# Performance work log

Measured on AMD Instinct MI355X. Metric: run time of the kernel, lower is better.

Reference implementation:

```python
import jax, jax.numpy as jnp
import numpy as np

N_NODES = 20000
N_EDGES = 320000
N_GRAPHS = 256
HIDDEN = 128
L = 4
NUM_ATOM = 28
NUM_BOND = 4
AVG_LOG = float(np.log(17.0))  # avg degree 16 -> avg_d['log']
EPS = 1e-5


def setup_inputs() -> dict:
    key = jax.random.key(0)
    ks = jax.random.split(key, 16)
    D = HIDDEN
    return {
        "x": jax.random.randint(ks[0], (N_NODES,), 0, NUM_ATOM, dtype=jnp.int32),
        "batch": jnp.sort(jax.random.randint(ks[1], (N_NODES,), 0, N_GRAPHS, dtype=jnp.int32)),
        "edge_index": jax.random.randint(ks[2], (2, N_EDGES), 0, N_NODES, dtype=jnp.int32),
        "snorm_n": jax.random.uniform(ks[3], (N_NODES, 1), dtype=jnp.float32),
        "edge_attr": jax.random.randint(ks[4], (N_EDGES,), 0, NUM_BOND, dtype=jnp.int32),
        "atom_emb": jax.random.normal(ks[5], (NUM_ATOM, D), jnp.float32) * 0.1,
        "bond_emb": jax.random.normal(ks[6], (NUM_BOND, D), jnp.float32) * 0.1,
        "pre_W": jax.random.normal(ks[7], (L, 3 * D, D), jnp.float32) / np.sqrt(3 * D),
        "pre_b": jnp.zeros((L, D), jnp.float32),
        "post_W": jax.random.normal(ks[8], (L, 13 * D, D), jnp.float32) / np.sqrt(13 * D),
        "post_b": jnp.zeros((L, D), jnp.float32),
        "mix_W": jax.random.normal(ks[9], (L, D, D), jnp.float32) / np.sqrt(D),
        "mix_b": jnp.zeros((L, D), jnp.float32),
        "bn_gamma": jnp.ones((L, D), jnp.float32),
        "bn_beta": jnp.zeros((L, D), jnp.float32),
        "r_W1": jax.random.normal(ks[10], (D, D // 2), jnp.float32) / np.sqrt(D),
        "r_b1": jnp.zeros((D // 2,), jnp.float32),
        "r_W2": jax.random.normal(ks[11], (D // 2, D // 4), jnp.float32) / np.sqrt(D // 2),
        "r_b2": jnp.zeros((D // 4,), jnp.float32),
        "r_W3": jax.random.normal(ks[12], (D // 4, 1), jnp.float32) / np.sqrt(D // 4),
        "r_b3": jnp.zeros((1,), jnp.float32),
    }


def _pna_forward(x, batch, edge_index, snorm_n, edge_attr,
                 atom_emb, bond_emb, pre_W, pre_b, post_W, post_b,
                 mix_W, mix_b, bn_gamma, bn_beta,
                 r_W1, r_b1, r_W2, r_b2, r_W3, r_b3):
    src, dst = edge_index[0], edge_index[1]
    h = atom_emb[x]                          # [N, D]
    e = bond_emb[edge_attr]                  # [E, D]
    # in-degree and PNA degree scalers (computed once)
    d = jax.ops.segment_sum(jnp.ones((src.shape[0],), h.dtype), dst, N_NODES)
    has_nb = (d > 0)[:, None]
    d_safe = jnp.maximum(d, 1.0)[:, None]
    logd = jnp.log1p(d)[:, None]
    amp = logd / AVG_LOG                     # amplification scaler
    att = AVG_LOG / jnp.maximum(logd, EPS)   # attenuation scaler
    for l in range(L):
        h_in = h
        # pretrans on edges: FC(cat(h_dst, h_src, e)) with LeakyReLU
        m = jnp.concatenate([h[dst], h[src], e], axis=-1)            # [E, 3D]
        m = jax.nn.leaky_relu(m @ pre_W[l] + pre_b[l])               # [E, D]
        # aggregators: mean, max, min, std
        mean = jax.ops.segment_sum(m, dst, N_NODES) / d_safe
        mean_sq = jax.ops.segment_sum(m * m, dst, N_NODES) / d_safe
        std = jnp.where(has_nb, jnp.sqrt(jax.nn.relu(mean_sq - mean * mean) + EPS), 0.0)
        mx = jnp.where(has_nb, jax.ops.segment_max(m, dst, N_NODES), 0.0)
        mn = jnp.where(has_nb, jax.ops.segment_min(m, dst, N_NODES), 0.0)
        agg = jnp.concatenate([mean, mx, mn, std], axis=-1)          # [N, 4D]
        agg = jnp.concatenate([agg, agg * amp, agg * att], axis=-1)  # [N, 12D]
        # posttrans FC on cat(h, agg) + mixing FC
        ph = jax.nn.leaky_relu(jnp.concatenate([h, agg], axis=-1) @ post_W[l] + post_b[l])
        ph = jax.nn.leaky_relu(ph @ mix_W[l] + mix_b[l])
        ph = ph * snorm_n                    # graph_norm
        mu = ph.mean(axis=0)                 # BatchNorm (training-mode stats)
        var = ph.var(axis=0)
        ph = bn_gamma[l] * (ph - mu) * jax.lax.rsqrt(var + EPS) + bn_beta[l]
        h = h_in + ph                        # residual
    # global mean pool per graph
    cnt = jax.ops.segment_sum(jnp.ones((x.shape[0],), h.dtype), batch, N_GRAPHS)
    g = jax.ops.segment_sum(h, batch, N_GRAPHS) / jnp.maximum(cnt, 1.0)[:, None]
    # MLPReadout: D -> D/2 -> D/4 -> 1 with ReLU
    g = jax.nn.relu(g @ r_W1 + r_b1)
    g = jax.nn.relu(g @ r_W2 + r_b2)
    return g @ r_W3 + r_b3                   # [B, 1]


def reference(x, batch, edge_index, snorm_n, edge_attr,
              atom_emb, bond_emb, pre_W, pre_b, post_W, post_b,
              mix_W, mix_b, bn_gamma, bn_beta,
              r_W1, r_b1, r_W2, r_b2, r_W3, r_b3):
    return _pna_forward(x, batch, edge_index, snorm_n, edge_attr,
                        atom_emb, bond_emb, pre_W, pre_b, post_W, post_b,
                        mix_W, mix_b, bn_gamma, bn_beta,
                        r_W1, r_b1, r_W2, r_b2, r_W3, r_b3)
```

## Files before the change

kernel.cpp:

```cpp
#include <hip/hip_runtime.h>
#include <math.h>

#define N_NODES 20000
#define N_EDGES 320000
#define N_GRAPHS 256
#define HID 128
#define NLAYERS 4
#define AVG_LOG 2.833213344056216f
#define EPS 1e-5f
#define MB64 313
#define NPAD 20032
#define SCANB 20
#define PITCH 40

typedef __attribute__((ext_vector_type(8))) short short8;
typedef __attribute__((ext_vector_type(4))) float f32x4;

static __device__ __forceinline__ float leaky(float v){ return v > 0.f ? v : 0.01f*v; }

static __device__ __forceinline__ void bsplit(float f, unsigned short& hi, unsigned short& lo){
  unsigned int u = __float_as_uint(f);
  unsigned int r = u + 0x7FFFu + ((u>>16)&1u);
  hi = (unsigned short)(r>>16);
  float hf = __uint_as_float(((unsigned int)hi)<<16);
  float l = f - hf;
  unsigned int v = __float_as_uint(l);
  unsigned int s = v + 0x7FFFu + ((v>>16)&1u);
  lo = (unsigned short)(s>>16);
}

static __device__ __forceinline__ void bsplit4(float4 f, ushort4& h, ushort4& l){
  bsplit(f.x, h.x, l.x); bsplit(f.y, h.y, l.y);
  bsplit(f.z, h.z, l.z); bsplit(f.w, h.w, l.w);
}

static __device__ __forceinline__ void gload16(const void* g, void* l){
  __builtin_amdgcn_global_load_lds((const __attribute__((address_space(1))) void*)g,
                                   (__attribute__((address_space(3))) void*)l, 16, 0, 0);
}

__global__ void k_count(const int* __restrict__ dst, int* __restrict__ deg){
  int e = blockIdx.x*blockDim.x + threadIdx.x;
  if (e < N_EDGES) atomicAdd(&deg[dst[e]], 1);
}

__global__ __launch_bounds__(1024) void k_scan1(const int* __restrict__ deg,
                                                int* __restrict__ excl, int* __restrict__ btot){
  __shared__ int buf[1024];
  int b = blockIdx.x, tid = threadIdx.x;
  int i = b*1024 + tid;
  int v = (i < N_NODES) ? deg[i] : 0;
  buf[tid] = v;
  __syncthreads();
  for (int ofs = 1; ofs < 1024; ofs <<= 1){
    int t = (tid >= ofs) ? buf[tid-ofs] : 0;
    __syncthreads();
    buf[tid] += t;
    __syncthreads();
  }
  excl[i] = buf[tid] - v;
  if (tid == 1023) btot[b] = buf[1023];
}

__global__ __launch_bounds__(1024) void k_scan2(
    const int* __restrict__ deg, const int* __restrict__ excl, const int* __restrict__ btot,
    int* __restrict__ off, float* __restrict__ invd,
    float* __restrict__ amp, float* __restrict__ att){
  __shared__ int carry_s;
  int b = blockIdx.x, tid = threadIdx.x;
  if (tid == 0){
    int c = 0;
    for (int j = 0; j < b; ++j) c += btot[j];
    carry_s = c;
  }
  __syncthreads();
  int i = b*1024 + tid;
  if (i <= N_NODES){
    off[i] = carry_s + excl[i];
    if (i < N_NODES){
      float d = (float)deg[i];
      invd[i] = 1.f / fmaxf(d, 1.f);
      float ld = log1pf(d);
      amp[i] = ld / AVG_LOG;
      att[i] = AVG_LOG / fmaxf(ld, EPS);
    }
  }
}

__global__ void k_fill(const int* __restrict__ src, const int* __restrict__ dst,
                       const int* __restrict__ eattr, const int* __restrict__ off,
                       int* __restrict__ cursor,
                       int* __restrict__ srcS, int* __restrict__ eaS){
  int e = blockIdx.x*blockDim.x + threadIdx.x;
  if (e < N_EDGES){
    int d = dst[e];
    int pos = off[d] + atomicAdd(&cursor[d], 1);
    srcS[pos] = src[e]; eaS[pos] = eattr[e];
  }
}

__global__ void k_goff(const int* __restrict__ batch, int* __restrict__ goff){
  int g = threadIdx.x;
  if (g <= N_GRAPHS){
    int lo = 0, hi = N_NODES;
    while (lo < hi){ int mid = (lo+hi)>>1; if (batch[mid] < g) lo = mid+1; else hi = mid; }
    goff[g] = lo;
  }
}

__global__ void k_hinit(const int* __restrict__ x, const float* __restrict__ atom_emb,
                        float* __restrict__ h,
                        unsigned short* __restrict__ h16h, unsigned short* __restrict__ h16l){
  int idx = blockIdx.x*blockDim.x + threadIdx.x;
  if (idx < N_NODES*32){
    int n = idx >> 5, q = idx & 31;
    float4 v = ((const float4*)atom_emb)[(size_t)x[n]*32 + q];
    ((float4*)h)[(size_t)n*32 + q] = v;
    ushort4 hh, ll; bsplit4(v, hh, ll);
    *(ushort4*)(h16h + (size_t)n*128 + q*4) = hh;
    *(ushort4*)(h16l + (size_t)n*128 + q*4) = ll;
  }
}

__global__ void k_bondall(const float* __restrict__ bond_emb, const float* __restrict__ pre_W,
                          const float* __restrict__ pre_b, float* __restrict__ BW3all){
  int l = blockIdx.x, tid = threadIdx.x;
  int r = tid >> 7, c = tid & 127;
  const float* W3 = pre_W + (size_t)l*384*128 + 256*128;
  float s = pre_b[l*128 + c];
  for (int k = 0; k < 128; ++k) s = fmaf(bond_emb[r*128 + k], W3[k*128 + c], s);
  BW3all[l*512 + tid] = s;
}

__global__ void k_wt(const float* __restrict__ pre_W, const float* __restrict__ post_W,
                     const float* __restrict__ mix_W,
                     unsigned short* __restrict__ whi, unsigned short* __restrict__ wlo){
  int y = blockIdx.y; int l = y/7, j = y%7;
  int K = (j>=3 && j<6) ? 512 : 128;
  const float* src; size_t off;
  if (j < 2)      { src = pre_W  + (size_t)l*384*128  + (size_t)j*128*128;            off = (size_t)j*16384; }
  else if (j == 2){ src = post_W + (size_t)l*1664*128;                                off = 2*16384; }
  else if (j < 6) { src = post_W + (size_t)l*1664*128 + (size_t)(128+(j-3)*512)*128;  off = 49152 + (size_t)(j-3)*65536; }
  else            { src = mix_W  + (size_t)l*128*128;                                 off = 245760; }
  unsigned short* dh = whi + (size_t)l*262144 + off;
  unsigned short* dl = wlo + (size_t)l*262144 + off;
  int kq8 = K/8;
  int ntask = 128*kq8;
  int t = blockIdx.x*256 + threadIdx.x;
  if (t >= ntask) return;
  int c  = t / kq8;
  int k0 = (t % kq8)*8;
  unsigned short h8[8] __attribute__((aligned(16)));
  unsigned short l8[8] __attribute__((aligned(16)));
  #pragma unroll
  for (int i=0;i<8;++i) bsplit(src[(size_t)(k0+i)*128 + c], h8[i], l8[i]);
  *(uint4*)(dh + (size_t)c*K + k0) = *(const uint4*)h8;
  *(uint4*)(dl + (size_t)c*K + k0) = *(const uint4*)l8;
}

template<int MODE>
__global__ __launch_bounds__(256) void k_mf16(
    const unsigned short* __restrict__ whi, const unsigned short* __restrict__ wlo,
    const unsigned short* __restrict__ Ahg, const unsigned short* __restrict__ Alg,
    float* __restrict__ out)
{
  const int K    = (MODE==1) ? 512 : 128;
  const int ASTR = (MODE==1) ? 512 : 128;
  const int OSTR = (MODE==1) ? 384 : 128;
  __shared__ unsigned short Ah[64*32], Al[64*32], Bh[128*32], Bl[128*32];
  int tid = threadIdx.x;
  int lane = tid & 63;
  int wv = tid >> 6;
  int wm = (wv>>1)*32, wn = (wv&1)*64;
  int y = blockIdx.x % 3;
  int mbase = (blockIdx.x / 3) * 64;
  const unsigned short* wh = whi + (size_t)y*K*128;
  const unsigned short* wl = wlo + (size_t)y*K*128;
  float* outp = out; int ocol = 0;
  if (MODE == 0) outp = out + (size_t)y*(size_t)N_NODES*128;
  if (MODE == 1) ocol = y*128;

  int lq = lane >> 2, ls = lane & 3;
  int kg = ls ^ (lq & 3) ^ ((lq >> 2) & 3);
  int a_row = wv*16 + lq;
  const unsigned short* agh = Ahg + (size_t)(mbase + a_row)*ASTR + kg*8;
  const unsigned short* agl = Alg + (size_t)(mbase + a_row)*ASTR + kg*8;
  unsigned short* a_ldsh = Ah + wv*512;
  unsigned short* a_ldsl = Al + wv*512;
  int b_col0 = (wv*2+0)*16 + lq;
  int b_col1 = (wv*2+1)*16 + lq;
  const unsigned short* bgh0 = wh + (size_t)b_col0*K + kg*8;
  const unsigned short* bgh1 = wh + (size_t)b_col1*K + kg*8;
  const unsigned short* bgl0 = wl + (size_t)b_col0*K + kg*8;
  const unsigned short* bgl1 = wl + (size_t)b_col1*K + kg*8;
  unsigned short* b_ldsh0 = Bh + (wv*2+0)*512;
  unsigned short* b_ldsh1 = Bh + (wv*2+1)*512;
  unsigned short* b_ldsl0 = Bl + (wv*2+0)*512;
  unsigned short* b_ldsl1 = Bl + (wv*2+1)*512;

  f32x4 acc[2][4];
  #pragma unroll
  for (int mi=0;mi<2;++mi)
    #pragma unroll
    for (int ni=0;ni<4;++ni)
      acc[mi][ni] = (f32x4){0.f,0.f,0.f,0.f};

  int lr = lane & 15, lk = lane >> 4;
  int sl = lk ^ (lr & 3) ^ ((lr >> 2) & 3);

  for (int kt = 0; kt < K; kt += 32){
    gload16(agh + kt, a_ldsh);
    gload16(agl + kt, a_ldsl);
    gload16(bgh0 + kt, b_ldsh0);
    gload16(bgh1 + kt, b_ldsh1);
    gload16(bgl0 + kt, b_ldsl0);
    gload16(bgl1 + kt, b_ldsl1);
    __syncthreads();
    short8 ah[2], al2[2], bh4[4], bl4[4];
    #pragma unroll
    for (int mi=0;mi<2;++mi){
      int idx = (wm + mi*16 + lr)*32 + sl*8;
      ah[mi]  = *(const short8*)(Ah + idx);
      al2[mi] = *(const short8*)(Al + idx);
    }
    #pragma unroll
    for (int ni=0;ni<4;++ni){
      int idx = (wn + ni*16 + lr)*32 + sl*8;
      bh4[ni] = *(const short8*)(Bh + idx);
      bl4[ni] = *(const short8*)(Bl + idx);
    }
    #pragma unroll
    for (int mi=0;mi<2;++mi){
      #pragma unroll
      for (int ni=0;ni<4;++ni){
        acc[mi][ni] = __builtin_amdgcn_mfma_f32_16x16x32_bf16(ah[mi],  bh4[ni], acc[mi][ni], 0,0,0);
        acc[mi][ni] = __builtin_amdgcn_mfma_f32_16x16x32_bf16(ah[mi],  bl4[ni], acc[mi][ni], 0,0,0);
        acc[mi][ni] = __builtin_amdgcn_mfma_f32_16x16x32_bf16(al2[mi], bh4[ni], acc[mi][ni], 0,0,0);
      }
    }
    __syncthreads();
  }

  #pragma unroll
  for (int mi=0;mi<2;++mi){
    #pragma unroll
    for (int ni=0;ni<4;++ni){
      int gcol = wn + ni*16 + lr;
      #pragma unroll
      for (int r=0;r<4;++r){
        int grow = mbase + wm + mi*16 + lk*4 + r;
        if (grow < N_NODES)
          outp[(size_t)grow*OSTR + ocol + gcol] = acc[mi][ni][r];
      }
    }
  }
}

__global__ __launch_bounds__(256) void k_mix(
    const unsigned short* __restrict__ wh, const unsigned short* __restrict__ wl,
    const float* __restrict__ Yh, const float* __restrict__ Yamt,
    const float* __restrict__ amp, const float* __restrict__ att,
    const float* __restrict__ post_b, const float* __restrict__ mix_b,
    const float* __restrict__ snorm,
    float* __restrict__ tb, float* __restrict__ bnpart)
{
  __shared__ unsigned short Ah[64*PITCH], Al[64*PITCH], Bh[128*PITCH], Bl[128*PITCH];
  __shared__ float bns[2][128], bnq[2][128];
  int tid = threadIdx.x;
  int lane = tid & 63;
  int wv = tid >> 6;
  int wm = (wv>>1)*32, wn = (wv&1)*64;
  int mbase = blockIdx.x*64;

  int a_row = tid >> 2, a_kg = tid & 3;
  int a_nrow = min(mbase + a_row, N_NODES-1);
  float av = amp[a_nrow], tv2 = att[a_nrow];
  const float* yhp = Yh   + (size_t)a_nrow*128;
  const float* yap = Yamt + (size_t)a_nrow*384;
  unsigned short* a_dh = Ah + a_row*PITCH + a_kg*8;
  unsigned short* a_dl = Al + a_row*PITCH + a_kg*8;

  f32x4 acc[2][4];
  #pragma unroll
  for (int mi=0;mi<2;++mi)
    #pragma unroll
    for (int ni=0;ni<4;++ni)
      acc[mi][ni] = (f32x4){0.f,0.f,0.f,0.f};

  int lr = lane & 15, lk = lane >> 4;

  for (int kt = 0; kt < 128; kt += 32){
    #pragma unroll
    for (int i=0;i<2;++i){
      int s = tid + 256*i;
      int col = s >> 2, kgg = s & 3;
      *(uint4*)(Bh + col*PITCH + kgg*8) = *(const uint4*)(wh + (size_t)col*128 + kt + kgg*8);
      *(uint4*)(Bl + col*PITCH + kgg*8) = *(const uint4*)(wl + (size_t)col*128 + kt + kgg*8);
    }
    {
      int c0 = kt + a_kg*8;
      float4 h0 = *(const float4*)(yhp + c0),       h1 = *(const float4*)(yhp + c0 + 4);
      float4 a0 = *(const float4*)(yap + c0),       a1 = *(const float4*)(yap + c0 + 4);
      float4 m0 = *(const float4*)(yap + 128 + c0), m1 = *(const float4*)(yap + 132 + c0);
      float4 t0 = *(const float4*)(yap + 256 + c0), t1 = *(const float4*)(yap + 260 + c0);
      float4 p0 = *(const float4*)(post_b + c0),    p1 = *(const float4*)(post_b + c0 + 4);
      float fv[8];
      fv[0] = leaky(h0.x + a0.x + av*m0.x + tv2*t0.x + p0.x);
      fv[1] = leaky(h0.y + a0.y + av*m0.y + tv2*t0.y + p0.y);
      fv[2] = leaky(h0.z + a0.z + av*m0.z + tv2*t0.z + p0.z);
      fv[3] = leaky(h0.w + a0.w + av*m0.w + tv2*t0.w + p0.w);
      fv[4] = leaky(h1.x + a1.x + av*m1.x + tv2*t1.x + p1.x);
      fv[5] = leaky(h1.y + a1.y + av*m1.y + tv2*t1.y + p1.y);
      fv[6] = leaky(h1.z + a1.z + av*m1.z + tv2*t1.z + p1.z);
      fv[7] = leaky(h1.w + a1.w + av*m1.w + tv2*t1.w + p1.w);
      unsigned short h8[8] __attribute__((aligned(16)));
      unsigned short l8[8] __attribute__((aligned(16)));
      #pragma unroll
      for (int i=0;i<8;++i) bsplit(fv[i], h8[i], l8[i]);
      *(uint4*)a_dh = *(const uint4*)h8;
      *(uint4*)a_dl = *(const uint4*)l8;
    }
    __syncthreads();
    short8 ah[2], al2[2], bh4[4], bl4[4];
    #pragma unroll
    for (int mi=0;mi<2;++mi){
      int idx = (wm + mi*16 + lr)*PITCH + lk*8;
      ah[mi]  = *(const short8*)(Ah + idx);
      al2[mi] = *(const short8*)(Al + idx);
    }
    #pragma unroll
    for (int ni=0;ni<4;++ni){
      int idx = (wn + ni*16 + lr)*PITCH + lk*8;
      bh4[ni] = *(const short8*)(Bh + idx);
      bl4[ni] = *(const short8*)(Bl + idx);
    }
    #pragma unroll
    for (int mi=0;mi<2;++mi){
      #pragma unroll
      for (int ni=0;ni<4;++ni){
        acc[mi][ni] = __builtin_amdgcn_mfma_f32_16x16x32_bf16(ah[mi],  bh4[ni], acc[mi][ni], 0,0,0);
        acc[mi][ni] = __builtin_amdgcn_mfma_f32_16x16x32_bf16(ah[mi],  bl4[ni], acc[mi][ni], 0,0,0);
        acc[mi][ni] = __builtin_amdgcn_mfma_f32_16x16x32_bf16(al2[mi], bh4[ni], acc[mi][ni], 0,0,0);
      }
    }
    __syncthreads();
  }

  float sn[2][4]; bool vld[2][4];
  #pragma unroll
  for (int mi=0;mi<2;++mi)
    #pragma unroll
    for (int r=0;r<4;++r){
      int grow = mbase + wm + mi*16 + lk*4 + r;
      vld[mi][r] = (grow < N_NODES);
      sn[mi][r] = vld[mi][r] ? snorm[grow] : 0.f;
    }
  int half = wv >> 1;
  #pragma unroll
  for (int ni=0;ni<4;++ni){
    int gcol = wn + ni*16 + lr;
    float bv = mix_b[gcol];
    float s = 0.f, q = 0.f;
    #pragma unroll
    for (int mi=0;mi<2;++mi){
      #pragma unroll
      for (int r=0;r<4;++r){
        if (vld[mi][r]){
          int grow = mbase + wm + mi*16 + lk*4 + r;
          float v = leaky(acc[mi][ni][r] + bv) * sn[mi][r];
          tb[(size_t)grow*128 + gcol] = v;
          s += v; q += v*v;
        }
      }
    }
    s += __shfl_xor(s, 16); s += __shfl_xor(s, 32);
    q += __shfl_xor(q, 16); q += __shfl_xor(q, 32);
    if (lk == 0){ bns[half][gcol] = s; bnq[half][gcol] = q; }
  }
  __syncthreads();
  if (tid < 128){
    bnpart[(size_t)blockIdx.x*256 + tid]       = bns[0][tid] + bns[1][tid];
    bnpart[(size_t)blockIdx.x*256 + 128 + tid] = bnq[0][tid] + bnq[1][tid];
  }
}

__global__ __launch_bounds__(256) void k_fusedagg(
    const float* __restrict__ H1, const float* __restrict__ H2,
    const float* __restrict__ BW3,
    const int* __restrict__ srcS, const int* __restrict__ eaS,
    const int* __restrict__ off, const float* __restrict__ invd,
    unsigned short* __restrict__ aggh, unsigned short* __restrict__ aggl)
{
  __shared__ float bw[4][128];
  int tid = threadIdx.x;
  bw[tid>>7][tid&127]     = BW3[tid];
  bw[2+(tid>>7)][tid&127] = BW3[256+tid];
  __syncthreads();

  int node = blockIdx.x*8 + (tid>>5);
  int q = tid & 31;
  float4 c4 = ((const float4*)(H1 + (size_t)node*HID))[q];
  int s = off[node], e = off[node+1];
  float4 sum = make_float4(0,0,0,0), sq = make_float4(0,0,0,0);
  float4 mx = make_float4(-3.4e38f,-3.4e38f,-3.4e38f,-3.4e38f);
  float4 mn = make_float4( 3.4e38f, 3.4e38f, 3.4e38f, 3.4e38f);

  #define FA_BODY(T,B) { \
    float vx = leaky(c4.x + T.x + B.x); \
    float vy = leaky(c4.y + T.y + B.y); \
    float vz = leaky(c4.z + T.z + B.z); \
    float vw = leaky(c4.w + T.w + B.w); \
    sum.x += vx; sum.y += vy; sum.z += vz; sum.w += vw; \
    sq.x += vx*vx; sq.y += vy*vy; sq.z += vz*vz; sq.w += vw*vw; \
    mx.x = fmaxf(mx.x, vx); mx.y = fmaxf(mx.y, vy); mx.z = fmaxf(mx.z, vz); mx.w = fmaxf(mx.w, vw); \
    mn.x = fminf(mn.x, vx); mn.y = fminf(mn.y, vy); mn.z = fminf(mn.z, vz); mn.w = fminf(mn.w, vw); }

  int i = s;
  for (; i + 1 < e; i += 2){
    int sv0 = srcS[i],   ev0 = eaS[i];
    int sv1 = srcS[i+1], ev1 = eaS[i+1];
    float4 t0 = ((const float4*)(H2 + (size_t)sv0*HID))[q];
    float4 t1 = ((const float4*)(H2 + (size_t)sv1*HID))[q];
    float4 b0 = ((const float4*)(&bw[ev0][0]))[q];
    float4 b1 = ((const float4*)(&bw[ev1][0]))[q];
    FA_BODY(t0,b0)
    FA_BODY(t1,b1)
  }
  if (i < e){
    int sv = srcS[i], ev = eaS[i];
    float4 t  = ((const float4*)(H2 + (size_t)sv*HID))[q];
    float4 b4 = ((const float4*)(&bw[ev][0]))[q];
    FA_BODY(t,b4)
  }
  #undef FA_BODY

  bool has = (e > s);
  float iv = invd[node];
  float4 mean = make_float4(sum.x*iv, sum.y*iv, sum.z*iv, sum.w*iv);
  float4 msq  = make_float4(sq.x*iv,  sq.y*iv,  sq.z*iv,  sq.w*iv);
  float4 sd;
  sd.x = has ? sqrtf(fmaxf(msq.x - mean.x*mean.x, 0.f) + EPS) : 0.f;
  sd.y = has ? sqrtf(fmaxf(msq.y - mean.y*mean.y, 0.f) + EPS) : 0.f;
  sd.z = has ? sqrtf(fmaxf(msq.z - mean.z*mean.z, 0.f) + EPS) : 0.f;
  sd.w = has ? sqrtf(fmaxf(msq.w - mean.w*mean.w, 0.f) + EPS) : 0.f;
  if (!has){ mx = make_float4(0,0,0,0); mn = make_float4(0,0,0,0); }
  size_t base = (size_t)node*512 + q*4;
  ushort4 hh, ll;
  bsplit4(mean, hh, ll);
  *(ushort4*)(aggh + base      ) = hh; *(ushort4*)(aggl + base      ) = ll;
  bsplit4(mx, hh, ll);
  *(ushort4*)(aggh + base + 128) = hh; *(ushort4*)(aggl + base + 128) = ll;
  bsplit4(mn, hh, ll);
  *(ushort4*)(aggh + base + 256) = hh; *(ushort4*)(aggl + base + 256) = ll;
  bsplit4(sd, hh, ll);
  *(ushort4*)(aggh + base + 384) = hh; *(ushort4*)(aggl + base + 384) = ll;
}

__global__ __launch_bounds__(512) void k_bnfinal(const float* __restrict__ bnpart,
                                                 float* __restrict__ mu, float* __restrict__ rstd){
  __shared__ double ss[4][128], qq[4][128];
  int tid = threadIdx.x;
  int c = tid & 127, p = tid >> 7;
  double s = 0.0, q = 0.0;
  for (int b = p; b < MB64; b += 4){
    s += (double)bnpart[(size_t)b*256 + c];
    q += (double)bnpart[(size_t)b*256 + 128 + c];
  }
  ss[p][c] = s; qq[p][c] = q;
  __syncthreads();
  if (p == 0){
    double S = ss[0][c] + ss[1][c] + ss[2][c] + ss[3][c];
    double Q = qq[0][c] + qq[1][c] + qq[2][c] + qq[3][c];
    double mean = S / (double)N_NODES;
    double var  = Q / (double)N_NODES - mean*mean;
    mu[c] = (float)mean;
    rstd[c] = rsqrtf((float)var + EPS);
  }
}

__global__ void k_apply(const float* __restrict__ t, const float* __restrict__ mu,
                        const float* __restrict__ rstd, const float* __restrict__ gamma,
                        const float* __restrict__ beta, float* __restrict__ h,
                        unsigned short* __restrict__ h16h, unsigned short* __restrict__ h16l){
  int idx = blockIdx.x*blockDim.x + threadIdx.x;
  if (idx < N_NODES*32){
    int n = idx >> 5, q = idx & 31;
    float4 tv = ((const float4*)t)[(size_t)n*32 + q];
    float4 hv = ((float4*)h)[(size_t)n*32 + q];
    float4 g4 = ((const float4*)gamma)[q], b4 = ((const float4*)beta)[q];
    float4 m4 = ((const float4*)mu)[q],    r4 = ((const float4*)rstd)[q];
    hv.x += g4.x*(tv.x-m4.x)*r4.x + b4.x;
    hv.y += g4.y*(tv.y-m4.y)*r4.y + b4.y;
    hv.z += g4.z*(tv.z-m4.z)*r4.z + b4.z;
    hv.w += g4.w*(tv.w-m4.w)*r4.w + b4.w;
    ((float4*)h)[(size_t)n*32 + q] = hv;
    ushort4 hh, ll; bsplit4(hv, hh, ll);
    *(ushort4*)(h16h + (size_t)n*128 + q*4) = hh;
    *(ushort4*)(h16l + (size_t)n*128 + q*4) = ll;
  }
}

__global__ __launch_bounds__(128) void k_poolread(
    const int* __restrict__ goff, const float* __restrict__ h,
    const float* __restrict__ W1, const float* __restrict__ b1,
    const float* __restrict__ W2, const float* __restrict__ b2,
    const float* __restrict__ W3, const float* __restrict__ b3,
    float* __restrict__ out){
  __shared__ float gl[128];
  __shared__ float a1[64];
  __shared__ float a2[32];
  int g = blockIdx.x, tid = threadIdx.x;
  int s = goff[g], e = goff[g+1];
  float sum = 0.f;
  for (int r = s; r < e; ++r) sum += h[(size_t)r*128 + tid];
  gl[tid] = sum / fmaxf((float)(e - s), 1.f);
  __syncthreads();
  if (tid < 64){
    float s1 = b1[tid];
    for (int k = 0; k < 128; ++k) s1 = fmaf(gl[k], W1[k*64 + tid], s1);
    a1[tid] = fmaxf(s1, 0.f);
  }
  __syncthreads();
  if (tid < 32){
    float s2 = b2[tid];
    for (int k = 0; k < 64; ++k) s2 = fmaf(a1[k], W2[k*32 + tid], s2);
    a2[tid] = fmaxf(s2, 0.f);
  }
  __syncthreads();
  if (tid == 0){
    float s3 = b3[0];
    for (int k = 0; k < 32; ++k) s3 = fmaf(a2[k], W3[k], s3);
    out[g] = s3;
  }
}

extern "C" void kernel_launch(void* const* d_in, const int* in_sizes, int n_in,
                              void* d_out, int out_size, void* d_ws, size_t ws_size,
                              hipStream_t stream) {
  const int*   x        = (const int*)  d_in[0];
  const int*   batch    = (const int*)  d_in[1];
  const int*   ei       = (const int*)  d_in[2];
  const float* snorm    = (const float*)d_in[3];
  const int*   eattr    = (const int*)  d_in[4];
  const float* atom_emb = (const float*)d_in[5];
  const float* bond_emb = (const float*)d_in[6];
  const float* pre_W    = (const float*)d_in[7];
  const float* pre_b    = (const float*)d_in[8];
  const float* post_W   = (const float*)d_in[9];
  const float* post_b   = (const float*)d_in[10];
  const float* mix_W    = (const float*)d_in[11];
  const float* mix_b    = (const float*)d_in[12];
  const float* bn_g     = (const float*)d_in[13];
  const float* bn_b     = (const float*)d_in[14];
  const float* rW1      = (const float*)d_in[15];
  const float* rb1      = (const float*)d_in[16];
  const float* rW2      = (const float*)d_in[17];
  const float* rb2      = (const float*)d_in[18];
  const float* rW3      = (const float*)d_in[19];
  const float* rb3      = (const float*)d_in[20];
  float* outp = (float*)d_out;

  const int* srcI = ei;
  const int* dstI = ei + N_EDGES;

  char* ws = (char*)d_ws;
  size_t o = 0;
  auto alloc = [&](size_t bytes)->char* {
    char* p = ws + o;
    o = (o + bytes + 255) & ~(size_t)255;
    return p;
  };
  int*    deg    = (int*)   alloc((size_t)N_NODES*4);
  int*    cursor = (int*)   alloc((size_t)N_NODES*4);
  int*    excl   = (int*)   alloc((size_t)SCANB*1024*4);
  int*    btot   = (int*)   alloc((size_t)SCANB*4);
  int*    off    = (int*)   alloc((size_t)(N_NODES+1)*4);
  int*    goff   = (int*)   alloc((size_t)(N_GRAPHS+1)*4);
  int*    srcS   = (int*)   alloc((size_t)N_EDGES*4);
  int*    eaS    = (int*)   alloc((size_t)N_EDGES*4);
  float*  invd   = (float*) alloc((size_t)N_NODES*4);
  float*  ampb   = (float*) alloc((size_t)N_NODES*4);
  float*  attb   = (float*) alloc((size_t)N_NODES*4);
  float*  h      = (float*) alloc((size_t)N_NODES*HID*4);
  float*  H3     = (float*) alloc((size_t)3*N_NODES*HID*4);
  float*  Yamt   = (float*) alloc((size_t)N_NODES*384*4);
  float*  BW3all = (float*) alloc((size_t)NLAYERS*512*4);
  float*  tb     = (float*) alloc((size_t)N_NODES*HID*4);
  unsigned short* whi  = (unsigned short*)alloc((size_t)NLAYERS*262144*2);
  unsigned short* wlo  = (unsigned short*)alloc((size_t)NLAYERS*262144*2);
  unsigned short* h16h = (unsigned short*)alloc((size_t)NPAD*128*2);
  unsigned short* h16l = (unsigned short*)alloc((size_t)NPAD*128*2);
  unsigned short* aggh = (unsigned short*)alloc((size_t)NPAD*512*2);
  unsigned short* aggl = (unsigned short*)alloc((size_t)NPAD*512*2);
  float*  bnpart = (float*) alloc((size_t)MB64*256*4);
  float*  mu     = (float*) alloc(128*4);
  float*  rstd   = (float*) alloc(128*4);

  hipMemsetAsync(deg, 0, (size_t)((char*)cursor - (char*)deg) + (size_t)N_NODES*4, stream);
  k_count<<<(N_EDGES+255)/256, 256, 0, stream>>>(dstI, deg);
  k_scan1<<<SCANB, 1024, 0, stream>>>(deg, excl, btot);
  k_scan2<<<SCANB, 1024, 0, stream>>>(deg, excl, btot, off, invd, ampb, attb);
  k_fill<<<(N_EDGES+255)/256, 256, 0, stream>>>(srcI, dstI, eattr, off, cursor, srcS, eaS);
  k_goff<<<1, 512, 0, stream>>>(batch, goff);
  k_hinit<<<(N_NODES*32+255)/256, 256, 0, stream>>>(x, atom_emb, h, h16h, h16l);
  k_wt<<<dim3(32, NLAYERS*7), 256, 0, stream>>>(pre_W, post_W, mix_W, whi, wlo);
  k_bondall<<<NLAYERS, 512, 0, stream>>>(bond_emb, pre_W, pre_b, BW3all);

  float* H1 = H3;
  float* H2 = H3 + (size_t)N_NODES*HID;
  float* Yh = H3 + (size_t)2*N_NODES*HID;
  for (int l = 0; l < NLAYERS; ++l){
    const unsigned short* whl = whi + (size_t)l*262144;
    const unsigned short* wll = wlo + (size_t)l*262144;
    k_mf16<0><<<MB64*3, 256, 0, stream>>>(whl, wll, h16h, h16l, H3);
    k_fusedagg<<<N_NODES/8, 256, 0, stream>>>(H1, H2, BW3all + (size_t)l*512,
        srcS, eaS, off, invd, aggh, aggl);
    k_mf16<1><<<MB64*3, 256, 0, stream>>>(whl + 49152, wll + 49152, aggh, aggl, Yamt);
    k_mix<<<MB64, 256, 0, stream>>>(whl + 245760, wll + 245760,
        Yh, Yamt, ampb, attb, post_b + (size_t)l*128, mix_b + (size_t)l*128,
        snorm, tb, bnpart);
    k_bnfinal<<<1, 512, 0, stream>>>(bnpart, mu, rstd);
    k_apply<<<(N_NODES*32+255)/256, 256, 0, stream>>>(tb, mu, rstd,
        bn_g + (size_t)l*128, bn_b + (size_t)l*128, h, h16h, h16l);
  }

  k_poolread<<<N_GRAPHS, 128, 0, stream>>>(goff, h, rW1, rb1, rW2, rb2, rW3, rb3, outp);
}
```

Before: 611.9 us.

## Fuse post-aggregation GEMM with mix GEMM into one per-tile kernel

Replaces the separate K=512 post GEMM (which wrote a 20000x384 fp32 Yamt buffer) and the mix GEMM kernel with a single k_post kernel over 32-row tiles. Each tile computes the three 128-column post outputs, combines them with amp/att scalers and leaky ReLU in registers, splits to bf16 hi/lo in LDS, then immediately runs the mix GEMM and writes BN partials. This removes the Yamt round trip and a launch. The cost is a smaller M tile, more blocks, larger LDS use that may lower occupancy, and weight tiles re-read per block.

```diff
diff --git a/kernel.cpp b/kernel.cpp
--- a/kernel.cpp
+++ b/kernel.cpp
@@ -9,9 +9,9 @@
 #define AVG_LOG 2.833213344056216f
 #define EPS 1e-5f
 #define MB64 313
+#define MBPOST 625
 #define NPAD 20032
 #define SCANB 20
-#define PITCH 40
 
 typedef __attribute__((ext_vector_type(8))) short short8;
 typedef __attribute__((ext_vector_type(4))) float f32x4;
@@ -158,15 +158,12 @@
   *(uint4*)(dl + (size_t)c*K + k0) = *(const uint4*)l8;
 }
 
-template<int MODE>
 __global__ __launch_bounds__(256) void k_mf16(
     const unsigned short* __restrict__ whi, const unsigned short* __restrict__ wlo,
     const unsigned short* __restrict__ Ahg, const unsigned short* __restrict__ Alg,
     float* __restrict__ out)
 {
-  const int K    = (MODE==1) ? 512 : 128;
-  const int ASTR = (MODE==1) ? 512 : 128;
-  const int OSTR = (MODE==1) ? 384 : 128;
+  const int K = 128;
   __shared__ unsigned short Ah[64*32], Al[64*32], Bh[128*32], Bl[128*32];
   int tid = threadIdx.x;
   int lane = tid & 63;
@@ -176,15 +173,13 @@
   int mbase = (blockIdx.x / 3) * 64;
   const unsigned short* wh = whi + (size_t)y*K*128;
   const unsigned short* wl = wlo + (size_t)y*K*128;
-  float* outp = out; int ocol = 0;
-  if (MODE == 0) outp = out + (size_t)y*(size_t)N_NODES*128;
-  if (MODE == 1) ocol = y*128;
+  float* outp = out + (size_t)y*(size_t)N_NODES*128;
 
   int lq = lane >> 2, ls = lane & 3;
   int kg = ls ^ (lq & 3) ^ ((lq >> 2) & 3);
   int a_row = wv*16 + lq;
-  const unsigned short* agh = Ahg + (size_t)(mbase + a_row)*ASTR + kg*8;
-  const unsigned short* agl = Alg + (size_t)(mbase + a_row)*ASTR + kg*8;
+  const unsigned short* agh = Ahg + (size_t)(mbase + a_row)*128 + kg*8;
+  const unsigned short* agl = Alg + (size_t)(mbase + a_row)*128 + kg*8;
   unsigned short* a_ldsh = Ah + wv*512;
   unsigned short* a_ldsl = Al + wv*512;
   int b_col0 = (wv*2+0)*16 + lq;
@@ -250,132 +245,157 @@
       for (int r=0;r<4;++r){
         int grow = mbase + wm + mi*16 + lk*4 + r;
         if (grow < N_NODES)
-          outp[(size_t)grow*OSTR + ocol + gcol] = acc[mi][ni][r];
+          outp[(size_t)grow*128 + gcol] = acc[mi][ni][r];
       }
     }
   }
 }
 
-__global__ __launch_bounds__(256) void k_mix(
-    const unsigned short* __restrict__ wh, const unsigned short* __restrict__ wl,
-    const float* __restrict__ Yh, const float* __restrict__ Yamt,
+__global__ __launch_bounds__(256) void k_post(
+    const unsigned short* __restrict__ whl, const unsigned short* __restrict__ wll,
+    const unsigned short* __restrict__ aggh, const unsigned short* __restrict__ aggl,
+    const float* __restrict__ Yh,
     const float* __restrict__ amp, const float* __restrict__ att,
     const float* __restrict__ post_b, const float* __restrict__ mix_b,
     const float* __restrict__ snorm,
     float* __restrict__ tb, float* __restrict__ bnpart)
 {
-  __shared__ unsigned short Ah[64*PITCH], Al[64*PITCH], Bh[128*PITCH], Bl[128*PITCH];
+  __shared__ unsigned short Ah[32*32], Al[32*32];
+  __shared__ unsigned short Bh[384*32], Bl[384*32];
+  __shared__ unsigned short Mh[128*32], Ml[128*32];
+  __shared__ float ampS[32], attS[32], pbS[128];
   __shared__ float bns[2][128], bnq[2][128];
-  int tid = threadIdx.x;
-  int lane = tid & 63;
-  int wv = tid >> 6;
-  int wm = (wv>>1)*32, wn = (wv&1)*64;
-  int mbase = blockIdx.x*64;
-
-  int a_row = tid >> 2, a_kg = tid & 3;
-  int a_nrow = min(mbase + a_row, N_NODES-1);
-  float av = amp[a_nrow], tv2 = att[a_nrow];
-  const float* yhp = Yh   + (size_t)a_nrow*128;
-  const float* yap = Yamt + (size_t)a_nrow*384;
-  unsigned short* a_dh = Ah + a_row*PITCH + a_kg*8;
-  unsigned short* a_dl = Al + a_row*PITCH + a_kg*8;
-
-  f32x4 acc[2][4];
+
+  int tid = threadIdx.x, lane = tid & 63, wv = tid >> 6;
+  int mbase = blockIdx.x * 32;
+  const unsigned short* wBh = whl + 49152;
+  const unsigned short* wBl = wll + 49152;
+  const unsigned short* wMh = whl + 245760;
+  const unsigned short* wMl = wll + 245760;
+
+  if (tid < 32)       ampS[tid]     = amp[mbase + tid];
+  else if (tid < 64)  attS[tid-32]  = att[mbase + tid - 32];
+  else if (tid < 192) pbS[tid-64]   = post_b[tid - 64];
+
+  int lq = lane >> 2, ls = lane & 3;
+  int kg = ls ^ (lq & 3) ^ ((lq >> 2) & 3);
+  int lr = lane & 15, lk = lane >> 4;
+  int sl = lk ^ (lr & 3) ^ ((lr >> 2) & 3);
+
+  const unsigned short* aSrc = ((wv < 2) ? aggh : aggl)
+        + (size_t)(mbase + (wv&1)*16 + lq)*512 + kg*8;
+  unsigned short* aDst = ((wv < 2) ? Ah : Al) + (wv&1)*16*32;
+
+  f32x4 acc1[3][2][2];
   #pragma unroll
-  for (int mi=0;mi<2;++mi)
-    #pragma unroll
-    for (int ni=0;ni<4;++ni)
-      acc[mi][ni] = (f32x4){0.f,0.f,0.f,0.f};
-
-  int lr = lane & 15, lk = lane >> 4;
-
-  for (int kt = 0; kt < 128; kt += 32){
-    #pragma unroll
-    for (int i=0;i<2;++i){
-      int s = tid + 256*i;
-      int col = s >> 2, kgg = s & 3;
-      *(uint4*)(Bh + col*PITCH + kgg*8) = *(const uint4*)(wh + (size_t)col*128 + kt + kgg*8);
-      *(uint4*)(Bl + col*PITCH + kgg*8) = *(const uint4*)(wl + (size_t)col*128 + kt + kgg*8);
-    }
-    {
-      int c0 = kt + a_kg*8;
-      float4 h0 = *(const float4*)(yhp + c0),       h1 = *(const float4*)(yhp + c0 + 4);
-      float4 a0 = *(const float4*)(yap + c0),       a1 = *(const float4*)(yap + c0 + 4);
-      float4 m0 = *(const float4*)(yap + 128 + c0), m1 = *(const float4*)(yap + 132 + c0);
-      float4 t0 = *(const float4*)(yap + 256 + c0), t1 = *(const float4*)(yap + 260 + c0);
-      float4 p0 = *(const float4*)(post_b + c0),    p1 = *(const float4*)(post_b + c0 + 4);
-      float fv[8];
-      fv[0] = leaky(h0.x + a0.x + av*m0.x + tv2*t0.x + p0.x);
-      fv[1] = leaky(h0.y + a0.y + av*m0.y + tv2*t0.y + p0.y);
-      fv[2] = leaky(h0.z + a0.z + av*m0.z + tv2*t0.z + p0.z);
-      fv[3] = leaky(h0.w + a0.w + av*m0.w + tv2*t0.w + p0.w);
-      fv[4] = leaky(h1.x + a1.x + av*m1.x + tv2*t1.x + p1.x);
-      fv[5] = leaky(h1.y + a1.y + av*m1.y + tv2*t1.y + p1.y);
-      fv[6] = leaky(h1.z + a1.z + av*m1.z + tv2*t1.z + p1.z);
-      fv[7] = leaky(h1.w + a1.w + av*m1.w + tv2*t1.w + p1.w);
-      unsigned short h8[8] __attribute__((aligned(16)));
-      unsigned short l8[8] __attribute__((aligned(16)));
+  for (int y=0;y<3;++y)
+    #pragma unroll
+    for (int ri=0;ri<2;++ri)
       #pragma unroll
-      for (int i=0;i<8;++i) bsplit(fv[i], h8[i], l8[i]);
-      *(uint4*)a_dh = *(const uint4*)h8;
-      *(uint4*)a_dl = *(const uint4*)l8;
-    }
-    __syncthreads();
-    short8 ah[2], al2[2], bh4[4], bl4[4];
-    #pragma unroll
-    for (int mi=0;mi<2;++mi){
-      int idx = (wm + mi*16 + lr)*PITCH + lk*8;
-      ah[mi]  = *(const short8*)(Ah + idx);
-      al2[mi] = *(const short8*)(Al + idx);
-    }
-    #pragma unroll
-    for (int ni=0;ni<4;++ni){
-      int idx = (wn + ni*16 + lr)*PITCH + lk*8;
-      bh4[ni] = *(const short8*)(Bh + idx);
-      bl4[ni] = *(const short8*)(Bl + idx);
-    }
-    #pragma unroll
-    for (int mi=0;mi<2;++mi){
+      for (int ci=0;ci<2;++ci)
+        acc1[y][ri][ci] = (f32x4){0.f,0.f,0.f,0.f};
+
+  for (int kt = 0; kt < 512; kt += 32){
+    gload16(aSrc + kt, aDst);
+    #pragma unroll
+    for (int i=0;i<6;++i){
+      int cb = wv*6 + i;
+      gload16(wBh + (size_t)(cb*16 + lq)*512 + kt + kg*8, Bh + cb*16*32);
+      gload16(wBl + (size_t)(cb*16 + lq)*512 + kt + kg*8, Bl + cb*16*32);
+    }
+    __syncthreads();
+    short8 a8h[2], a8l[2];
+    #pragma unroll
+    for (int ri=0;ri<2;++ri){
+      int idx = (ri*16 + lr)*32 + sl*8;
+      a8h[ri] = *(const short8*)(Ah + idx);
+      a8l[ri] = *(const short8*)(Al + idx);
+    }
+    #pragma unroll
+    for (int y=0;y<3;++y){
+      short8 b8h[2], b8l[2];
       #pragma unroll
-      for (int ni=0;ni<4;++ni){
-        acc[mi][ni] = __builtin_amdgcn_mfma_f32_16x16x32_bf16(ah[mi],  bh4[ni], acc[mi][ni], 0,0,0);
-        acc[mi][ni] = __builtin_amdgcn_mfma_f32_16x16x32_bf16(ah[mi],  bl4[ni], acc[mi][ni], 0,0,0);
-        acc[mi][ni] = __builtin_amdgcn_mfma_f32_16x16x32_bf16(al2[mi], bh4[ni], acc[mi][ni], 0,0,0);
+      for (int ci=0;ci<2;++ci){
+        int row = y*128 + wv*32 + ci*16 + lr;
+        b8h[ci] = *(const short8*)(Bh + row*32 + sl*8);
+        b8l[ci] = *(const short8*)(Bl + row*32 + sl*8);
       }
-    }
-    __syncthreads();
-  }
-
-  float sn[2][4]; bool vld[2][4];
-  #pragma unroll
-  for (int mi=0;mi<2;++mi)
-    #pragma unroll
-    for (int r=0;r<4;++r){
-      int grow = mbase + wm + mi*16 + lk*4 + r;
-      vld[mi][r] = (grow < N_NODES);
-      sn[mi][r] = vld[mi][r] ? snorm[grow] : 0.f;
-    }
-  int half = wv >> 1;
-  #pragma unroll
-  for (int ni=0;ni<4;++ni){
-    int gcol = wn + ni*16 + lr;
-    float bv = mix_b[gcol];
-    float s = 0.f, q = 0.f;
-    #pragma unroll
-    for (int mi=0;mi<2;++mi){
       #pragma unroll
-      for (int r=0;r<4;++r){
-        if (vld[mi][r]){
-          int grow = mbase + wm + mi*16 + lk*4 + r;
-          float v = leaky(acc[mi][ni][r] + bv) * sn[mi][r];
-          tb[(size_t)grow*128 + gcol] = v;
-          s += v; q += v*v;
+      for (int ri=0;ri<2;++ri){
+        #pragma unroll
+        for (int ci=0;ci<2;++ci){
+          acc1[y][ri][ci] = __builtin_amdgcn_mfma_f32_16x16x32_bf16(a8h[ri], b8h[ci], acc1[y][ri][ci], 0,0,0);
+          acc1[y][ri][ci] = __builtin_amdgcn_mfma_f32_16x16x32_bf16(a8h[ri], b8l[ci], acc1[y][ri][ci], 0,0,0);
+          acc1[y][ri][ci] = __builtin_amdgcn_mfma_f32_16x16x32_bf16(a8l[ri], b8h[ci], acc1[y][ri][ci], 0,0,0);
         }
       }
     }
+    __syncthreads();
+  }
+
+  #pragma unroll
+  for (int ri=0;ri<2;++ri){
+    #pragma unroll
+    for (int ci=0;ci<2;++ci){
+      int cc = wv*32 + ci*16 + lr;
+      float pb = pbS[cc];
+      #pragma unroll
+      for (int j=0;j<4;++j){
+        int rl = ri*16 + lk*4 + j;
+        float yv = Yh[(size_t)(mbase + rl)*128 + cc];
+        float v = leaky(yv + acc1[0][ri][ci][j] + ampS[rl]*acc1[1][ri][ci][j]
+                           + attS[rl]*acc1[2][ri][ci][j] + pb);
+        unsigned short hh, ll; bsplit(v, hh, ll);
+        Bh[rl*136 + cc] = hh;
+        Bl[rl*136 + cc] = ll;
+      }
+    }
+  }
+  __syncthreads();
+
+  f32x4 acc2[4];
+  #pragma unroll
+  for (int ci=0;ci<4;++ci) acc2[ci] = (f32x4){0.f,0.f,0.f,0.f};
+  int r4 = 16*(wv>>1);
+  int c4 = 64*(wv&1);
+
+  for (int kt = 0; kt < 128; kt += 32){
+    #pragma unroll
+    for (int i=0;i<2;++i){
+      int cb = wv*2 + i;
+      gload16(wMh + (size_t)(cb*16 + lq)*128 + kt + kg*8, Mh + cb*16*32);
+      gload16(wMl + (size_t)(cb*16 + lq)*128 + kt + kg*8, Ml + cb*16*32);
+    }
+    __syncthreads();
+    short8 ph8 = *(const short8*)(Bh + (r4 + lr)*136 + kt + lk*8);
+    short8 pl8 = *(const short8*)(Bl + (r4 + lr)*136 + kt + lk*8);
+    #pragma unroll
+    for (int ci=0;ci<4;++ci){
+      int mrow = c4 + ci*16 + lr;
+      short8 mh8 = *(const short8*)(Mh + mrow*32 + sl*8);
+      short8 ml8 = *(const short8*)(Ml + mrow*32 + sl*8);
+      acc2[ci] = __builtin_amdgcn_mfma_f32_16x16x32_bf16(ph8, mh8, acc2[ci], 0,0,0);
+      acc2[ci] = __builtin_amdgcn_mfma_f32_16x16x32_bf16(ph8, ml8, acc2[ci], 0,0,0);
+      acc2[ci] = __builtin_amdgcn_mfma_f32_16x16x32_bf16(pl8, mh8, acc2[ci], 0,0,0);
+    }
+    __syncthreads();
+  }
+
+  #pragma unroll
+  for (int ci=0;ci<4;++ci){
+    int col = c4 + ci*16 + lr;
+    float mbv = mix_b[col];
+    float s = 0.f, q = 0.f;
+    #pragma unroll
+    for (int j=0;j<4;++j){
+      int row = mbase + r4 + lk*4 + j;
+      float v = leaky(acc2[ci][j] + mbv) * snorm[row];
+      tb[(size_t)row*128 + col] = v;
+      s += v; q += v*v;
+    }
     s += __shfl_xor(s, 16); s += __shfl_xor(s, 32);
     q += __shfl_xor(q, 16); q += __shfl_xor(q, 32);
-    if (lk == 0){ bns[half][gcol] = s; bnq[half][gcol] = q; }
+    if (lk == 0){ bns[wv>>1][col] = s; bnq[wv>>1][col] = q; }
   }
   __syncthreads();
   if (tid < 128){
@@ -462,7 +482,7 @@
   int tid = threadIdx.x;
   int c = tid & 127, p = tid >> 7;
   double s = 0.0, q = 0.0;
-  for (int b = p; b < MB64; b += 4){
+  for (int b = p; b < MBPOST; b += 4){
     s += (double)bnpart[(size_t)b*256 + c];
     q += (double)bnpart[(size_t)b*256 + 128 + c];
   }
@@ -583,7 +603,6 @@
   float*  attb   = (float*) alloc((size_t)N_NODES*4);
   float*  h      = (float*) alloc((size_t)N_NODES*HID*4);
   float*  H3     = (float*) alloc((size_t)3*N_NODES*HID*4);
-  float*  Yamt   = (float*) alloc((size_t)N_NODES*384*4);
   float*  BW3all = (float*) alloc((size_t)NLAYERS*512*4);
   float*  tb     = (float*) alloc((size_t)N_NODES*HID*4);
   unsigned short* whi  = (unsigned short*)alloc((size_t)NLAYERS*262144*2);
@@ -592,7 +611,7 @@
   unsigned short* h16l = (unsigned short*)alloc((size_t)NPAD*128*2);
   unsigned short* aggh = (unsigned short*)alloc((size_t)NPAD*512*2);
   unsigned short* aggl = (unsigned short*)alloc((size_t)NPAD*512*2);
-  float*  bnpart = (float*) alloc((size_t)MB64*256*4);
+  float*  bnpart = (float*) alloc((size_t)MBPOST*256*4);
   float*  mu     = (float*) alloc(128*4);
   float*  rstd   = (float*) alloc(128*4);
 
@@ -612,12 +631,11 @@
   for (int l = 0; l < NLAYERS; ++l){
     const unsigned short* whl = whi + (size_t)l*262144;
     const unsigned short* wll = wlo + (size_t)l*262144;
-    k_mf16<0><<<MB64*3, 256, 0, stream>>>(whl, wll, h16h, h16l, H3);
+    k_mf16<<<MB64*3, 256, 0, stream>>>(whl, wll, h16h, h16l, H3);
     k_fusedagg<<<N_NODES/8, 256, 0, stream>>>(H1, H2, BW3all + (size_t)l*512,
         srcS, eaS, off, invd, aggh, aggl);
-    k_mf16<1><<<MB64*3, 256, 0, stream>>>(whl + 49152, wll + 49152, aggh, aggl, Yamt);
-    k_mix<<<MB64, 256, 0, stream>>>(whl + 245760, wll + 245760,
-        Yh, Yamt, ampb, attb, post_b + (size_t)l*128, mix_b + (size_t)l*128,
+    k_post<<<MBPOST, 256, 0, stream>>>(whl, wll, aggh, aggl, Yh,
+        ampb, attb, post_b + (size_t)l*128, mix_b + (size_t)l*128,
         snorm, tb, bnpart);
     k_bnfinal<<<1, 512, 0, stream>>>(bnpart, mu, rstd);
     k_apply<<<(N_NODES*32+255)/256, 256, 0, stream>>>(tb, mu, rstd,
```

Result: slower. 731.0 us (+19.5%).
